# Optimization experiments

Hardware: AMD Instinct MI355X
Metric: run time of the kernel (lower is better)

## Reference

```python
import jax, jax.numpy as jnp
import numpy as np

CHEB_K = 3

def avwgcn(x, E, W_pool, b_pool):
    # x: [B,N,Cin], E: [N,e], W_pool: [e,K,Cin,Cout], b_pool: [e,Cout]
    N = E.shape[0]
    A = jax.nn.softmax(jax.nn.relu(E @ E.T), axis=1)          # adaptive adjacency [N,N]
    supports = [jnp.eye(N, dtype=x.dtype), A]
    for _ in range(2, CHEB_K):
        supports.append(2.0 * (A @ supports[-1]) - supports[-2])
    S = jnp.stack(supports)                                    # [K,N,N]
    W = jnp.einsum('ne,ekio->nkio', E, W_pool)                 # per-node weights
    b = E @ b_pool                                             # [N,Cout]
    xg = jnp.einsum('knm,bmi->bnki', S, x)                     # Chebyshev graph conv
    return jnp.einsum('bnki,nkio->bno', xg, W) + b


def setup_inputs() -> dict:
    key = jax.random.key(0)
    ks = jax.random.split(key, 7)
    B, N, Din, Dout, E_DIM = 64, 1024, 64, 64, 16
    C = Din + Dout
    return {
        'x': jax.random.normal(ks[0], (B, N, Din), dtype=jnp.float32),
        'state': jax.random.normal(ks[1], (B, N, Dout), dtype=jnp.float32),
        'node_embeddings': jax.random.normal(ks[2], (N, E_DIM), dtype=jnp.float32),
        'gate_W_pool': jax.random.normal(ks[3], (E_DIM, CHEB_K, C, 2 * Dout), dtype=jnp.float32) * 0.1,
        'gate_b_pool': jax.random.normal(ks[4], (E_DIM, 2 * Dout), dtype=jnp.float32) * 0.1,
        'upd_W_pool': jax.random.normal(ks[5], (E_DIM, CHEB_K, C, Dout), dtype=jnp.float32) * 0.1,
        'upd_b_pool': jax.random.normal(ks[6], (E_DIM, Dout), dtype=jnp.float32) * 0.1,
    }


def reference(x, state, node_embeddings, gate_W_pool, gate_b_pool, upd_W_pool, upd_b_pool):
    hidden_dim = state.shape[-1]
    input_and_state = jnp.concatenate([x, state], axis=-1)
    z_r = jax.nn.sigmoid(avwgcn(input_and_state, node_embeddings, gate_W_pool, gate_b_pool))
    z, r = z_r[..., :hidden_dim], z_r[..., hidden_dim:]
    candidate = jnp.concatenate([x, z * state], axis=-1)
    hc = jnp.tanh(avwgcn(candidate, node_embeddings, upd_W_pool, upd_b_pool))
    return r * state + (1.0 - r) * hc
```

## Files before the change

kernel.cpp:

```cpp
#include <hip/hip_runtime.h>
#include <math.h>

#define N_NODES 1024
#define B_SZ 64
#define GNH 4096
#define KI 384
#define EDIM 16

typedef _Float16 half8_t __attribute__((ext_vector_type(8)));
typedef float f32x4 __attribute__((ext_vector_type(4)));

__device__ __forceinline__ unsigned short f2h(float f) {
    _Float16 h = (_Float16)f;
    return *(unsigned short*)&h;
}
__device__ __forceinline__ float h2f(unsigned short u) {
    _Float16 h = *(_Float16*)&u;
    return (float)h;
}
__device__ __forceinline__ float sigmoidf_(float v) {
    return 1.f / (1.f + __expf(-v));
}
__device__ __forceinline__ void load_lds16(const void* g, void* l) {
    __builtin_amdgcn_global_load_lds(
        (const __attribute__((address_space(1))) void*)g,
        (__attribute__((address_space(3))) void*)l, 16, 0, 0);
}

__global__ __launch_bounds__(256) void compute_A_kernel(
    const float* __restrict__ E, unsigned short* __restrict__ Ah) {
    __shared__ float red[256];
    const int tid = threadIdx.x;
    const int n = blockIdx.x;
    float en[EDIM];
#pragma unroll
    for (int e = 0; e < EDIM; ++e) en[e] = E[n * EDIM + e];
    float logit[4], lmax = -1e30f;
#pragma unroll
    for (int j = 0; j < 4; ++j) {
        const int m = tid + j * 256;
        float d = 0.f;
#pragma unroll
        for (int e = 0; e < EDIM; ++e) d += en[e] * E[m * EDIM + e];
        d = fmaxf(d, 0.f);
        logit[j] = d;
        lmax = fmaxf(lmax, d);
    }
    red[tid] = lmax;
    __syncthreads();
    for (int s = 128; s > 0; s >>= 1) {
        if (tid < s) red[tid] = fmaxf(red[tid], red[tid + s]);
        __syncthreads();
    }
    lmax = red[0];
    __syncthreads();
    float ex[4], lsum = 0.f;
#pragma unroll
    for (int j = 0; j < 4; ++j) {
        ex[j] = __expf(logit[j] - lmax);
        lsum += ex[j];
    }
    red[tid] = lsum;
    __syncthreads();
    for (int s = 128; s > 0; s >>= 1) {
        if (tid < s) red[tid] += red[tid + s];
        __syncthreads();
    }
    const float inv = 1.f / red[0];
#pragma unroll
    for (int j = 0; j < 4; ++j)
        Ah[n * N_NODES + tid + j * 256] = f2h(ex[j] * inv);
}

__global__ __launch_bounds__(256) void build_T0_all_kernel(
    const float* __restrict__ x, const float* __restrict__ state,
    unsigned short* __restrict__ TX0, unsigned short* __restrict__ TS0,
    unsigned short* __restrict__ TX0T, unsigned short* __restrict__ TS0T) {
    __shared__ unsigned short Lx[64 * 72];
    __shared__ unsigned short Lss[64 * 72];
    const int tid = threadIdx.x;
    const int n0 = blockIdx.x * 64;
    const int b = blockIdx.y;
#pragma unroll
    for (int t = 0; t < 16; ++t) {
        const int id = t * 256 + tid;
        const int nl = id >> 6;
        const int c = id & 63;
        const float xv = x[((size_t)b * N_NODES + n0 + nl) * 64 + c];
        const float sv = state[((size_t)b * N_NODES + n0 + nl) * 64 + c];
        const unsigned short xh = f2h(xv), sh = f2h(sv);
        TX0[(size_t)(n0 + nl) * GNH + b * 64 + c] = xh;
        TS0[(size_t)(n0 + nl) * GNH + b * 64 + c] = sh;
        Lx[c * 72 + nl] = xh;
        Lss[c * 72 + nl] = sh;
    }
    __syncthreads();
#pragma unroll
    for (int t = 0; t < 2; ++t) {
        const int id = t * 256 + tid;
        const int c = id >> 3;
        const int n8 = id & 7;
        uint4 xv = *(const uint4*)&Lx[c * 72 + n8 * 8];
        uint4 sv = *(const uint4*)&Lss[c * 72 + n8 * 8];
        *(uint4*)&TX0T[(size_t)(b * 64 + c) * N_NODES + n0 + n8 * 8] = xv;
        *(uint4*)&TS0T[(size_t)(b * 64 + c) * N_NODES + n0 + n8 * 8] = sv;
    }
}

__global__ __launch_bounds__(256) void transpose16_kernel(
    const unsigned short* __restrict__ src, unsigned short* __restrict__ dst,
    int W) {
    __shared__ unsigned short Ls[64 * 72];
    const int tid = threadIdx.x;
    const int r0 = blockIdx.x * 64;
    const int c0 = blockIdx.y * 64;
#pragma unroll
    for (int t = 0; t < 2; ++t) {
        const int id = t * 256 + tid;
        const int row = id >> 3;
        const int c8 = id & 7;
        uint4 v = *(const uint4*)&src[(size_t)(r0 + row) * W + c0 + c8 * 8];
        const unsigned short* vp = (const unsigned short*)&v;
#pragma unroll
        for (int j = 0; j < 8; ++j) Ls[(c8 * 8 + j) * 72 + row] = vp[j];
    }
    __syncthreads();
#pragma unroll
    for (int t = 0; t < 2; ++t) {
        const int id = t * 256 + tid;
        const int c = id >> 3;
        const int r8 = id & 7;
        uint4 v = *(const uint4*)&Ls[c * 72 + r8 * 8];
        *(uint4*)&dst[(size_t)(c0 + c) * N_NODES + r0 + r8 * 8] = v;
    }
}

__global__ __launch_bounds__(256) void gemm_s2_kernel(
    const unsigned short* __restrict__ Ah,
    const unsigned short* __restrict__ AhT, unsigned short* __restrict__ S2h) {
    __shared__ unsigned short As[64 * 64];
    __shared__ unsigned short Bs[64 * 64];
    const int tid = threadIdx.x;
    const int wave = tid >> 6;
    const int lane = tid & 63;
    const int l15 = lane & 15;
    const int quad = lane >> 4;
    const int n0 = blockIdx.x * 64;
    const int m0 = blockIdx.y * 64;
    const int wn = wave * 16;
    const int lr = lane >> 3;
    const int lsw = (lane & 7) ^ lr;

    f32x4 acc[4] = {};
    for (int k0 = 0; k0 < N_NODES; k0 += 64) {
#pragma unroll
        for (int i = 0; i < 2; ++i) {
            const int rbase = (wave * 2 + i) * 8;
            load_lds16(&Ah[(size_t)(n0 + rbase + lr) * N_NODES + k0 + lsw * 8],
                       &As[rbase * 64]);
            load_lds16(&AhT[(size_t)(m0 + rbase + lr) * N_NODES + k0 + lsw * 8],
                       &Bs[rbase * 64]);
        }
        __syncthreads();
#pragma unroll
        for (int ks = 0; ks < 2; ++ks) {
            const int slot = ((ks * 4 + quad) ^ (l15 & 7)) * 8;
            const half8_t b = *(const half8_t*)&Bs[(wn + l15) * 64 + slot];
#pragma unroll
            for (int mi = 0; mi < 4; ++mi) {
                const half8_t a = *(const half8_t*)&As[(mi * 16 + l15) * 64 + slot];
                acc[mi] =
                    __builtin_amdgcn_mfma_f32_16x16x32_f16(a, b, acc[mi], 0, 0, 0);
            }
        }
        __syncthreads();
    }
#pragma unroll
    for (int mi = 0; mi < 4; ++mi) {
#pragma unroll
        for (int r = 0; r < 4; ++r) {
            const int n_g = n0 + mi * 16 + quad * 4 + r;
            const int m_g = m0 + wn + l15;
            const float v = 2.f * acc[mi][r] - (n_g == m_g ? 1.f : 0.f);
            S2h[(size_t)n_g * N_NODES + m_g] = f2h(v);
        }
    }
}

__global__ __launch_bounds__(256) void gemm_graph_kernel(
    const unsigned short* __restrict__ Ah,
    const unsigned short* __restrict__ S2h,
    const unsigned short* __restrict__ BTX,
    const unsigned short* __restrict__ BTS,
    unsigned short* __restrict__ T1X, unsigned short* __restrict__ T1S,
    unsigned short* __restrict__ T2X, unsigned short* __restrict__ T2S,
    int ysplit, int colsPerXcd) {
    __shared__ union {
        struct {
            unsigned short As[128 * 64];
            unsigned short Bs[128 * 64];
        } s;
        unsigned short Cs[64 * 136];
    } lds;
    const int tid = threadIdx.x;
    const int wave = tid >> 6;
    const int lane = tid & 63;
    const int l15 = lane & 15;
    const int quad = lane >> 4;
    const int wm = (wave >> 1) * 64;
    const int wn = (wave & 1) * 64;
    const int id = blockIdx.x;
    const int xcd = id & 7;
    const int j = id >> 3;
    const int mrow0 = (j & 15) * 128;
    const int ytile = xcd * colsPerXcd + (j >> 4);
    const bool isA = mrow0 < N_NODES;
    const unsigned short* Asrc =
        (isA ? Ah : S2h) + (size_t)(mrow0 & 1023) * N_NODES;
    const bool isX = ytile < ysplit;
    const int col0 = (isX ? ytile : ytile - ysplit) * 128;
    const unsigned short* Bsrc =
        (isX ? BTX : BTS) + (size_t)col0 * N_NODES;
    unsigned short* OUT =
        (isA ? (isX ? T1X : T1S) : (isX ? T2X : T2S)) +
        (size_t)(mrow0 & 1023) * GNH + col0;
    const int lr = lane >> 3;
    const int lsw = (lane & 7) ^ lr;

    f32x4 acc[4][4] = {};

    for (int k0 = 0; k0 < N_NODES; k0 += 64) {
#pragma unroll
        for (int i = 0; i < 4; ++i) {
            const int rbase = (wave * 4 + i) * 8;
            load_lds16(&Asrc[(size_t)(rbase + lr) * N_NODES + k0 + lsw * 8],
                       &lds.s.As[rbase * 64]);
        }
#pragma unroll
        for (int i = 0; i < 4; ++i) {
            const int rbase = (wave * 4 + i) * 8;
            load_lds16(&Bsrc[(size_t)(rbase + lr) * N_NODES + k0 + lsw * 8],
                       &lds.s.Bs[rbase * 64]);
        }
        __syncthreads();
#pragma unroll
        for (int ks = 0; ks < 2; ++ks) {
            const int slot = ((ks * 4 + quad) ^ (l15 & 7)) * 8;
            half8_t a[4], b[4];
#pragma unroll
            for (int mi = 0; mi < 4; ++mi)
                a[mi] = *(const half8_t*)&lds.s
                             .As[(wm + mi * 16 + l15) * 64 + slot];
#pragma unroll
            for (int ni = 0; ni < 4; ++ni)
                b[ni] = *(const half8_t*)&lds.s
                             .Bs[(wn + ni * 16 + l15) * 64 + slot];
#pragma unroll
            for (int mi = 0; mi < 4; ++mi)
#pragma unroll
                for (int ni = 0; ni < 4; ++ni)
                    acc[mi][ni] = __builtin_amdgcn_mfma_f32_16x16x32_f16(
                        a[mi], b[ni], acc[mi][ni], 0, 0, 0);
        }
        __syncthreads();
    }

#pragma unroll
    for (int p = 0; p < 2; ++p) {
        if (p) __syncthreads();
        if ((wave >> 1) == p) {
#pragma unroll
            for (int mi = 0; mi < 4; ++mi)
#pragma unroll
                for (int ni = 0; ni < 4; ++ni)
#pragma unroll
                    for (int r = 0; r < 4; ++r) {
                        const int row = mi * 16 + quad * 4 + r;
                        const int col = wn + ni * 16 + l15;
                        lds.Cs[row * 136 + col] = f2h(acc[mi][ni][r]);
                    }
        }
        __syncthreads();
#pragma unroll
        for (int i = 0; i < 4; ++i) {
            const int id2 = i * 256 + tid;
            const int row = id2 >> 4;
            const int c8 = id2 & 15;
            uint4 cv = *(const uint4*)&lds.Cs[row * 136 + c8 * 8];
            *(uint4*)&OUT[(size_t)(p * 64 + row) * GNH + c8 * 8] = cv;
        }
    }
}

__global__ __launch_bounds__(256) void dequant_kernel(
    const float* __restrict__ Wp, const float* __restrict__ E,
    unsigned short* __restrict__ Wt, int NO) {
    __shared__ float En[32 * 16];
    const int tid = threadIdx.x;
    const int ki0 = blockIdx.x * 32;
    const int o0 = blockIdx.y * 32;
    const int n0 = blockIdx.z * 32;
    const int o = tid >> 3;
    const int k4 = tid & 7;

#pragma unroll
    for (int t = 0; t < 2; ++t) {
        const int id = t * 256 + tid;
        En[id] = E[(n0 + (id >> 4)) * EDIM + (id & 15)];
    }
    __syncthreads();

    f32x4 w[EDIM];
#pragma unroll
    for (int e = 0; e < EDIM; ++e) {
        f32x4 v;
#pragma unroll
        for (int j = 0; j < 4; ++j)
            v[j] = Wp[(size_t)(e * KI + ki0 + k4 * 4 + j) * NO + o0 + o];
        w[e] = v;
    }

    const size_t wt_base = ((size_t)n0 * NO + (o0 + o)) * KI + ki0 + k4 * 4;
#pragma unroll 4
    for (int nl = 0; nl < 32; ++nl) {
        f32x4 a = {0.f, 0.f, 0.f, 0.f};
#pragma unroll
        for (int e = 0; e < EDIM; ++e) a += w[e] * En[nl * EDIM + e];
        union { unsigned short u[4]; uint2 v; } pk;
#pragma unroll
        for (int j = 0; j < 4; ++j) pk.u[j] = f2h(a[j]);
        *(uint2*)&Wt[wt_base + (size_t)nl * NO * KI] = pk.v;
    }
}

__global__ __launch_bounds__(256) void pernode_gate_kernel(
    const unsigned short* __restrict__ TX0,
    const unsigned short* __restrict__ TS0,
    const unsigned short* __restrict__ TX1,
    const unsigned short* __restrict__ TS1,
    const unsigned short* __restrict__ TX2,
    const unsigned short* __restrict__ TS2,
    const unsigned short* __restrict__ Wt, const float* __restrict__ E,
    const float* __restrict__ bp, const float* __restrict__ state,
    unsigned short* __restrict__ rbuf, unsigned short* __restrict__ ts0_out) {
    __shared__ unsigned short XsX[64 * 64];
    __shared__ unsigned short XsS[64 * 64];
    const int n = blockIdx.x;
    const int tid = threadIdx.x;
    const int wave = tid >> 6;
    const int lane = tid & 63;
    const int l15 = lane & 15;
    const int quad = lane >> 4;
    const int wn = wave * 32;
    const int lr = lane >> 3;
    const int lsw = (lane & 7) ^ lr;

    float bias[2];
#pragma unroll
    for (int ni = 0; ni < 2; ++ni) {
        float bv = 0.f;
#pragma unroll
        for (int e = 0; e < EDIM; ++e)
            bv += E[n * EDIM + e] * bp[e * 128 + wn + ni * 16 + l15];
        bias[ni] = bv;
    }

    f32x4 acc[4][2] = {};

    const unsigned short* TXs[3] = {TX0, TX1, TX2};
    const unsigned short* TSs[3] = {TS0, TS1, TS2};
    const unsigned short* wrow0 = Wt + ((size_t)n * 128 + wn + l15) * KI;
    const unsigned short* wrow1 = Wt + ((size_t)n * 128 + wn + 16 + l15) * KI;

    for (int s = 0; s < 3; ++s) {
        const unsigned short* xs = TXs[s] + (size_t)n * GNH;
        const unsigned short* ss = TSs[s] + (size_t)n * GNH;
#pragma unroll
        for (int i = 0; i < 2; ++i) {
            const int slab = wave * 2 + i;
            load_lds16(xs + (slab * 8 + lr) * 64 + lsw * 8, &XsX[slab * 512]);
            load_lds16(ss + (slab * 8 + lr) * 64 + lsw * 8, &XsS[slab * 512]);
        }
        __syncthreads();
#pragma unroll
        for (int ks = 0; ks < 4; ++ks) {
            const int kseg = ks * 4 + quad;
            half8_t b[2];
            b[0] = *(const half8_t*)&wrow0[s * 128 + kseg * 8];
            b[1] = *(const half8_t*)&wrow1[s * 128 + kseg * 8];
            const unsigned short* plane = (kseg < 8) ? XsX : XsS;
            const int aslot = ((kseg & 7) ^ (l15 & 7)) * 8;
#pragma unroll
            for (int mi = 0; mi < 4; ++mi) {
                const half8_t a =
                    *(const half8_t*)&plane[(mi * 16 + l15) * 64 + aslot];
#pragma unroll
                for (int ni = 0; ni < 2; ++ni)
                    acc[mi][ni] = __builtin_amdgcn_mfma_f32_16x16x32_f16(
                        a, b[ni], acc[mi][ni], 0, 0, 0);
            }
        }
        __syncthreads();
    }

#pragma unroll
    for (int mi = 0; mi < 4; ++mi) {
#pragma unroll
        for (int r = 0; r < 4; ++r) {
            const int b_g = mi * 16 + quad * 4 + r;
#pragma unroll
            for (int ni = 0; ni < 2; ++ni) {
                const int o_g = wn + ni * 16 + l15;
                const float v = sigmoidf_(acc[mi][ni][r] + bias[ni]);
                if (o_g < 64) {
                    const float sv =
                        state[((size_t)b_g * N_NODES + n) * 64 + o_g];
                    ts0_out[(size_t)n * GNH + b_g * 64 + o_g] = f2h(v * sv);
                } else {
                    rbuf[((size_t)n * B_SZ + b_g) * 64 + (o_g - 64)] = f2h(v);
                }
            }
        }
    }
}

__global__ __launch_bounds__(256) void pernode_upd_kernel(
    const unsigned short* __restrict__ TX0,
    const unsigned short* __restrict__ TS0,
    const unsigned short* __restrict__ TX1,
    const unsigned short* __restrict__ TS1,
    const unsigned short* __restrict__ TX2,
    const unsigned short* __restrict__ TS2,
    const unsigned short* __restrict__ Wt, const float* __restrict__ E,
    const float* __restrict__ bp, const float* __restrict__ state,
    const unsigned short* __restrict__ rbuf, float* __restrict__ out) {
    __shared__ unsigned short XsX[64 * 64];
    __shared__ unsigned short XsS[64 * 64];
    const int n = blockIdx.x;
    const int tid = threadIdx.x;
    const int wave = tid >> 6;
    const int lane = tid & 63;
    const int l15 = lane & 15;
    const int quad = lane >> 4;
    const int wn = wave * 16;
    const int o_g = wn + l15;
    const int lr = lane >> 3;
    const int lsw = (lane & 7) ^ lr;

    float bias = 0.f;
#pragma unroll
    for (int e = 0; e < EDIM; ++e)
        bias += E[n * EDIM + e] * bp[e * 64 + o_g];

    f32x4 acc[4] = {};

    const unsigned short* TXs[3] = {TX0, TX1, TX2};
    const unsigned short* TSs[3] = {TS0, TS1, TS2};
    const unsigned short* wrow = Wt + ((size_t)n * 64 + o_g) * KI;

    for (int s = 0; s < 3; ++s) {
        const unsigned short* xs = TXs[s] + (size_t)n * GNH;
        const unsigned short* ss = TSs[s] + (size_t)n * GNH;
#pragma unroll
        for (int i = 0; i < 2; ++i) {
            const int slab = wave * 2 + i;
            load_lds16(xs + (slab * 8 + lr) * 64 + lsw * 8, &XsX[slab * 512]);
            load_lds16(ss + (slab * 8 + lr) * 64 + lsw * 8, &XsS[slab * 512]);
        }
        __syncthreads();
#pragma unroll
        for (int ks = 0; ks < 4; ++ks) {
            const int kseg = ks * 4 + quad;
            const half8_t b = *(const half8_t*)&wrow[s * 128 + kseg * 8];
            const unsigned short* plane = (kseg < 8) ? XsX : XsS;
            const int aslot = ((kseg & 7) ^ (l15 & 7)) * 8;
#pragma unroll
            for (int mi = 0; mi < 4; ++mi) {
                const half8_t a =
                    *(const half8_t*)&plane[(mi * 16 + l15) * 64 + aslot];
                acc[mi] = __builtin_amdgcn_mfma_f32_16x16x32_f16(a, b, acc[mi],
                                                                 0, 0, 0);
            }
        }
        __syncthreads();
    }

#pragma unroll
    for (int mi = 0; mi < 4; ++mi) {
#pragma unroll
        for (int r = 0; r < 4; ++r) {
            const int b_g = mi * 16 + quad * 4 + r;
            const float hc = tanhf(acc[mi][r] + bias);
            const float rr = h2f(rbuf[((size_t)n * B_SZ + b_g) * 64 + o_g]);
            const float sv = state[((size_t)b_g * N_NODES + n) * 64 + o_g];
            out[((size_t)b_g * N_NODES + n) * 64 + o_g] =
                rr * sv + (1.f - rr) * hc;
        }
    }
}

extern "C" void kernel_launch(void* const* d_in, const int* in_sizes, int n_in,
                              void* d_out, int out_size, void* d_ws,
                              size_t ws_size, hipStream_t stream) {
    const float* x = (const float*)d_in[0];
    const float* state = (const float*)d_in[1];
    const float* E = (const float*)d_in[2];
    const float* gW = (const float*)d_in[3];
    const float* gb = (const float*)d_in[4];
    const float* uW = (const float*)d_in[5];
    const float* ub = (const float*)d_in[6];
    float* out = (float*)d_out;

    char* ws = (char*)d_ws;
    unsigned short* Ah = (unsigned short*)ws;
    unsigned short* AhT = (unsigned short*)(ws + 2097152);
    unsigned short* S2h = (unsigned short*)(ws + 4194304);
    unsigned short* TX0 = (unsigned short*)(ws + 6291456);
    unsigned short* TS0 = (unsigned short*)(ws + 14680064);
    unsigned short* TX0T = (unsigned short*)(ws + 23068672);
    unsigned short* TS0T = (unsigned short*)(ws + 31457280);
    unsigned short* TX1 = (unsigned short*)(ws + 39845888);
    unsigned short* TS1 = (unsigned short*)(ws + 48234496);
    unsigned short* TX2 = (unsigned short*)(ws + 56623104);
    unsigned short* TS2 = (unsigned short*)(ws + 65011712);
    unsigned short* Wt = (unsigned short*)(ws + 73400320);
    unsigned short* rbuf = (unsigned short*)(ws + 174063616);

    compute_A_kernel<<<N_NODES, 256, 0, stream>>>(E, Ah);
    build_T0_all_kernel<<<dim3(16, 64), 256, 0, stream>>>(x, state, TX0, TS0,
                                                          TX0T, TS0T);
    transpose16_kernel<<<dim3(16, 16), 256, 0, stream>>>(Ah, AhT, N_NODES);
    gemm_s2_kernel<<<dim3(16, 16), 256, 0, stream>>>(Ah, AhT, S2h);

    gemm_graph_kernel<<<1024, 256, 0, stream>>>(
        Ah, S2h, TX0T, TS0T, TX1, TS1, TX2, TS2, 32, 8);
    dequant_kernel<<<dim3(12, 4, 32), 256, 0, stream>>>(gW, E, Wt, 128);
    pernode_gate_kernel<<<N_NODES, 256, 0, stream>>>(
        TX0, TS0, TX1, TS1, TX2, TS2, Wt, E, gb, state, rbuf, TS0);
    transpose16_kernel<<<dim3(16, 64), 256, 0, stream>>>(TS0, TS0T, GNH);

    gemm_graph_kernel<<<512, 256, 0, stream>>>(
        Ah, S2h, TX0T, TS0T, TX1, TS1, TX2, TS2, 0, 4);
    dequant_kernel<<<dim3(12, 2, 32), 256, 0, stream>>>(uW, E, Wt, 64);
    pernode_upd_kernel<<<N_NODES, 256, 0, stream>>>(
        TX0, TS0, TX1, TS1, TX2, TS2, Wt, E, ub, state, rbuf, out);
}
```

Baseline: 309.3 us.

## Rewrite graph GEMM with 8-wave larger tiles and 4-slot async LDS pipeline

After: 293.2 us. 1.05x faster.

```diff
diff --git a/kernel.cpp b/kernel.cpp
--- a/kernel.cpp
+++ b/kernel.cpp
@@ -187,7 +187,8 @@
     }
 }
 
-__global__ __launch_bounds__(256) void gemm_graph_kernel(
+template <int BM>
+__global__ __launch_bounds__(512, 2) void gemm_graph8_kernel(
     const unsigned short* __restrict__ Ah,
     const unsigned short* __restrict__ S2h,
     const unsigned short* __restrict__ BTX,
@@ -195,80 +196,152 @@
     unsigned short* __restrict__ T1X, unsigned short* __restrict__ T1S,
     unsigned short* __restrict__ T2X, unsigned short* __restrict__ T2S,
     int ysplit, int colsPerXcd) {
-    __shared__ union {
-        struct {
-            unsigned short As[128 * 64];
-            unsigned short Bs[128 * 64];
-        } s;
-        unsigned short Cs[64 * 136];
-    } lds;
+    constexpr int MFR = BM / 32;
+    constexpr int ASLOT_H = BM * 32;
+    constexpr int SLOT_H = ASLOT_H + 8192;
+    constexpr int APASS = BM / 128;
+    constexpr int MT = 2048 / BM;
+    __shared__ unsigned short lds[4 * SLOT_H];
+
     const int tid = threadIdx.x;
     const int wave = tid >> 6;
     const int lane = tid & 63;
     const int l15 = lane & 15;
     const int quad = lane >> 4;
-    const int wm = (wave >> 1) * 64;
-    const int wn = (wave & 1) * 64;
+    const int wm = (wave >> 2) * (BM / 2);
+    const int wn = (wave & 3) * 64;
+
     const int id = blockIdx.x;
     const int xcd = id & 7;
     const int j = id >> 3;
-    const int mrow0 = (j & 15) * 128;
-    const int ytile = xcd * colsPerXcd + (j >> 4);
+    const int mtile = j & (MT - 1);
+    const int ytile = xcd * colsPerXcd + j / MT;
+    const int mrow0 = mtile * BM;
     const bool isA = mrow0 < N_NODES;
     const unsigned short* Asrc =
         (isA ? Ah : S2h) + (size_t)(mrow0 & 1023) * N_NODES;
     const bool isX = ytile < ysplit;
-    const int col0 = (isX ? ytile : ytile - ysplit) * 128;
-    const unsigned short* Bsrc =
-        (isX ? BTX : BTS) + (size_t)col0 * N_NODES;
-    unsigned short* OUT =
-        (isA ? (isX ? T1X : T1S) : (isX ? T2X : T2S)) +
-        (size_t)(mrow0 & 1023) * GNH + col0;
-    const int lr = lane >> 3;
-    const int lsw = (lane & 7) ^ lr;
-
-    f32x4 acc[4][4] = {};
-
-    for (int k0 = 0; k0 < N_NODES; k0 += 64) {
-#pragma unroll
-        for (int i = 0; i < 4; ++i) {
-            const int rbase = (wave * 4 + i) * 8;
-            load_lds16(&Asrc[(size_t)(rbase + lr) * N_NODES + k0 + lsw * 8],
-                       &lds.s.As[rbase * 64]);
-        }
-#pragma unroll
-        for (int i = 0; i < 4; ++i) {
-            const int rbase = (wave * 4 + i) * 8;
-            load_lds16(&Bsrc[(size_t)(rbase + lr) * N_NODES + k0 + lsw * 8],
-                       &lds.s.Bs[rbase * 64]);
-        }
-        __syncthreads();
-#pragma unroll
-        for (int ks = 0; ks < 2; ++ks) {
-            const int slot = ((ks * 4 + quad) ^ (l15 & 7)) * 8;
-            half8_t a[4], b[4];
-#pragma unroll
-            for (int mi = 0; mi < 4; ++mi)
-                a[mi] = *(const half8_t*)&lds.s
-                             .As[(wm + mi * 16 + l15) * 64 + slot];
-#pragma unroll
-            for (int ni = 0; ni < 4; ++ni)
-                b[ni] = *(const half8_t*)&lds.s
-                             .Bs[(wn + ni * 16 + l15) * 64 + slot];
-#pragma unroll
-            for (int mi = 0; mi < 4; ++mi)
-#pragma unroll
-                for (int ni = 0; ni < 4; ++ni)
-                    acc[mi][ni] = __builtin_amdgcn_mfma_f32_16x16x32_f16(
-                        a[mi], b[ni], acc[mi][ni], 0, 0, 0);
-        }
-        __syncthreads();
-    }
-
-#pragma unroll
-    for (int p = 0; p < 2; ++p) {
-        if (p) __syncthreads();
-        if ((wave >> 1) == p) {
+    const int col0 = (isX ? ytile : ytile - ysplit) * 256;
+    const unsigned short* Bsrc = (isX ? BTX : BTS) + (size_t)col0 * N_NODES;
+    unsigned short* OUT = (isA ? (isX ? T1X : T1S) : (isX ? T2X : T2S)) +
+                          (size_t)(mrow0 & 1023) * GNH + col0;
+
+    int goff[2];
+#pragma unroll
+    for (int jp = 0; jp < 2; ++jp) {
+        const int cell = jp * 512 + tid;
+        const int prow = cell >> 3;
+        const int q = (cell & 7) ^ (prow & 7);
+        goff[jp] = (2 * prow + (q >> 2)) * N_NODES + (q & 3) * 8;
+    }
+
+    int offA[MFR], offB[4];
+#pragma unroll
+    for (int mi = 0; mi < MFR; ++mi) {
+        const int prow = (wm >> 1) + mi * 8 + (l15 >> 1);
+        const int s8 = ((l15 & 1) * 4 + quad) ^ (prow & 7);
+        offA[mi] = prow * 64 + s8 * 8;
+    }
+#pragma unroll
+    for (int ni = 0; ni < 4; ++ni) {
+        const int pcol = (wn >> 1) + ni * 8 + (l15 >> 1);
+        const int s8 = ((l15 & 1) * 4 + quad) ^ (pcol & 7);
+        offB[ni] = ASLOT_H + pcol * 64 + s8 * 8;
+    }
+
+    f32x4 acc[MFR][4] = {};
+
+    auto stageA = [&](int t) {
+        const int sl = t & 3;
+#pragma unroll
+        for (int jp = 0; jp < APASS; ++jp)
+            load_lds16(Asrc + (size_t)t * 32 + goff[jp],
+                       &lds[sl * SLOT_H + jp * 4096 + wave * 512]);
+    };
+    auto stageB = [&](int t) {
+        const int sl = t & 3;
+#pragma unroll
+        for (int jp = 0; jp < 2; ++jp)
+            load_lds16(Bsrc + (size_t)t * 32 + goff[jp],
+                       &lds[sl * SLOT_H + ASLOT_H + jp * 4096 + wave * 512]);
+    };
+    auto waitPipe = [&] {
+        if constexpr (BM == 256)
+            asm volatile("s_waitcnt vmcnt(8)" ::: "memory");
+        else
+            asm volatile("s_waitcnt vmcnt(6)" ::: "memory");
+    };
+
+    auto tileBody = [&](int t, bool tail) {
+        const unsigned short* base = &lds[(t & 3) * SLOT_H];
+        half8_t a[MFR], b0, b1, b2, b3;
+#pragma unroll
+        for (int mi = 0; mi < MFR; ++mi)
+            a[mi] = *(const half8_t*)&base[offA[mi]];
+        b0 = *(const half8_t*)&base[offB[0]];
+        b1 = *(const half8_t*)&base[offB[1]];
+        if (!tail) stageA(t + 3);
+        __builtin_amdgcn_sched_barrier(0);
+        __builtin_amdgcn_s_barrier();
+        asm volatile("s_waitcnt lgkmcnt(0)" ::: "memory");
+        __builtin_amdgcn_sched_barrier(0);
+        __builtin_amdgcn_s_setprio(1);
+#pragma unroll
+        for (int mi = 0; mi < MFR; ++mi) {
+            acc[mi][0] = __builtin_amdgcn_mfma_f32_16x16x32_f16(
+                a[mi], b0, acc[mi][0], 0, 0, 0);
+            acc[mi][1] = __builtin_amdgcn_mfma_f32_16x16x32_f16(
+                a[mi], b1, acc[mi][1], 0, 0, 0);
+        }
+        __builtin_amdgcn_s_setprio(0);
+        __builtin_amdgcn_sched_barrier(0);
+        __builtin_amdgcn_s_barrier();
+        b2 = *(const half8_t*)&base[offB[2]];
+        b3 = *(const half8_t*)&base[offB[3]];
+        if (!tail) {
+            stageB(t + 3);
+            waitPipe();
+        } else {
+            asm volatile("s_waitcnt vmcnt(0)" ::: "memory");
+        }
+        __builtin_amdgcn_sched_barrier(0);
+        __builtin_amdgcn_s_barrier();
+        asm volatile("s_waitcnt lgkmcnt(0)" ::: "memory");
+        __builtin_amdgcn_sched_barrier(0);
+        __builtin_amdgcn_s_setprio(1);
+#pragma unroll
+        for (int mi = 0; mi < MFR; ++mi) {
+            acc[mi][2] = __builtin_amdgcn_mfma_f32_16x16x32_f16(
+                a[mi], b2, acc[mi][2], 0, 0, 0);
+            acc[mi][3] = __builtin_amdgcn_mfma_f32_16x16x32_f16(
+                a[mi], b3, acc[mi][3], 0, 0, 0);
+        }
+        __builtin_amdgcn_s_setprio(0);
+        __builtin_amdgcn_sched_barrier(0);
+        __builtin_amdgcn_s_barrier();
+    };
+
+    stageA(0); stageB(0);
+    stageA(1); stageB(1);
+    stageA(2); stageB(2);
+    waitPipe();
+    __builtin_amdgcn_s_barrier();
+    __builtin_amdgcn_sched_barrier(0);
+
+#pragma unroll 4
+    for (int t = 0; t < 28; ++t) tileBody(t, false);
+    tileBody(28, false);
+    tileBody(29, true);
+    tileBody(30, true);
+    tileBody(31, true);
+
+    constexpr int NPASS = BM / 64;
+#pragma unroll
+    for (int p = 0; p < NPASS; ++p) {
+        __syncthreads();
+        const int whalf = (BM == 256) ? (p >> 1) : p;
+        const int mi0 = (BM == 256) ? (p & 1) * 4 : 0;
+        if ((wave >> 2) == whalf) {
 #pragma unroll
             for (int mi = 0; mi < 4; ++mi)
 #pragma unroll
@@ -277,17 +350,17 @@
                     for (int r = 0; r < 4; ++r) {
                         const int row = mi * 16 + quad * 4 + r;
                         const int col = wn + ni * 16 + l15;
-                        lds.Cs[row * 136 + col] = f2h(acc[mi][ni][r]);
+                        lds[row * 264 + col] = f2h(acc[mi0 + mi][ni][r]);
                     }
         }
         __syncthreads();
 #pragma unroll
         for (int i = 0; i < 4; ++i) {
-            const int id2 = i * 256 + tid;
-            const int row = id2 >> 4;
-            const int c8 = id2 & 15;
-            uint4 cv = *(const uint4*)&lds.Cs[row * 136 + c8 * 8];
-            *(uint4*)&OUT[(size_t)(p * 64 + row) * GNH + c8 * 8] = cv;
+            const int id2 = i * 512 + tid;
+            const int row = id2 >> 5;
+            const int c8 = id2 & 31;
+            uint4 v = *(const uint4*)&lds[row * 264 + c8 * 8];
+            *(uint4*)&OUT[(size_t)(p * 64 + row) * GNH + c8 * 8] = v;
         }
     }
 }
@@ -532,15 +605,15 @@
     transpose16_kernel<<<dim3(16, 16), 256, 0, stream>>>(Ah, AhT, N_NODES);
     gemm_s2_kernel<<<dim3(16, 16), 256, 0, stream>>>(Ah, AhT, S2h);
 
-    gemm_graph_kernel<<<1024, 256, 0, stream>>>(
-        Ah, S2h, TX0T, TS0T, TX1, TS1, TX2, TS2, 32, 8);
+    gemm_graph8_kernel<256><<<256, 512, 0, stream>>>(
+        Ah, S2h, TX0T, TS0T, TX1, TS1, TX2, TS2, 16, 4);
     dequant_kernel<<<dim3(12, 4, 32), 256, 0, stream>>>(gW, E, Wt, 128);
     pernode_gate_kernel<<<N_NODES, 256, 0, stream>>>(
         TX0, TS0, TX1, TS1, TX2, TS2, Wt, E, gb, state, rbuf, TS0);
     transpose16_kernel<<<dim3(16, 64), 256, 0, stream>>>(TS0, TS0T, GNH);
 
-    gemm_graph_kernel<<<512, 256, 0, stream>>>(
-        Ah, S2h, TX0T, TS0T, TX1, TS1, TX2, TS2, 0, 4);
+    gemm_graph8_kernel<128><<<256, 512, 0, stream>>>(
+        Ah, S2h, TX0T, TS0T, TX1, TS1, TX2, TS2, 0, 2);
     dequant_kernel<<<dim3(12, 2, 32), 256, 0, stream>>>(uW, E, Wt, 64);
     pernode_upd_kernel<<<N_NODES, 256, 0, stream>>>(
         TX0, TS0, TX1, TS1, TX2, TS2, Wt, E, ub, state, rbuf, out);
```
